# Performance work log

Measured on AMD Instinct MI355X. Metric: run time of the kernel, lower is better.

The kernel has to match this reference:

```python
import jax, jax.numpy as jnp
import numpy as np

B, T, E = 2, 2048, 2048
H, HKV, D = 32, 8, 64
G = H // HKV  # groups = 4
ROPE_BASE = 10000.0


def setup_inputs() -> dict:
    key = jax.random.key(0)
    ks = jax.random.split(key, 5)
    s = 0.02
    return {
        "x": jax.random.normal(ks[0], (B, T, E), dtype=jnp.float32),
        "Wq": jax.random.normal(ks[1], (E, H * D), dtype=jnp.float32) * s,
        "Wk": jax.random.normal(ks[2], (E, HKV * D), dtype=jnp.float32) * s,
        "Wv": jax.random.normal(ks[3], (E, HKV * D), dtype=jnp.float32) * s,
        "Wo": jax.random.normal(ks[4], (E, E), dtype=jnp.float32) * s,
    }


def _rope_tables(t, d, dtype):
    # standard rotate-half RoPE, theta base 10000
    inv_freq = 1.0 / (ROPE_BASE ** (jnp.arange(0, d, 2, dtype=jnp.float32) / d))
    ang = jnp.arange(t, dtype=jnp.float32)[:, None] * inv_freq[None, :]  # [T, D/2]
    return jnp.cos(ang).astype(dtype), jnp.sin(ang).astype(dtype)


def _apply_rope(x, cos, sin):
    # x: [B, h, T, D]; cos/sin: [T, D/2]
    d2 = x.shape[-1] // 2
    x1, x2 = x[..., :d2], x[..., d2:]
    return jnp.concatenate([x1 * cos - x2 * sin, x2 * cos + x1 * sin], axis=-1)


def reference(x, Wq, Wk, Wv, Wo):
    b, t, _ = x.shape
    q = (x @ Wq).reshape(b, t, H, D).transpose(0, 2, 1, 3)      # [B,H,T,D]
    k = (x @ Wk).reshape(b, t, HKV, D).transpose(0, 2, 1, 3)    # [B,HKV,T,D]
    v = (x @ Wv).reshape(b, t, HKV, D).transpose(0, 2, 1, 3)    # [B,HKV,T,D]

    cos, sin = _rope_tables(t, D, x.dtype)
    q = _apply_rope(q, cos, sin)
    k = _apply_rope(k, cos, sin)

    # GQA: keep KV unexpanded, broadcast groups inside the contraction
    qg = q.reshape(b, HKV, G, t, D)
    scale = 1.0 / np.sqrt(D)
    scores = jnp.einsum('bkgtd,bksd->bkgts', qg, k) * scale      # [B,HKV,G,T,T]
    causal = jnp.tril(jnp.ones((t, t), dtype=bool))
    scores = jnp.where(causal, scores, jnp.finfo(scores.dtype).min)
    attn = jax.nn.softmax(scores, axis=-1)
    y = jnp.einsum('bkgts,bksd->bkgtd', attn, v)                 # [B,HKV,G,T,D]
    y = y.reshape(b, H, t, D).transpose(0, 2, 1, 3).reshape(b, t, H * D)
    return y @ Wo
```

## Files before the change

### kernel.cpp

```cpp
#include <hip/hip_runtime.h>
#include <hip/hip_bf16.h>
#include <cstdint>
#include <cstddef>

typedef __bf16 bf16;
typedef __attribute__((ext_vector_type(8))) __bf16 bf16x8;
typedef __attribute__((ext_vector_type(4))) __bf16 bf16x4v;
typedef __attribute__((ext_vector_type(4))) float f32x4;

#define NB 2
#define NT 2048
#define NE 2048
#define NH 32
#define NHKV 8
#define ND 64
#define NBT (NB * NT)
#define NQKV 3072

__device__ __forceinline__ void gload_lds16(const void* g, void* l) {
  __builtin_amdgcn_global_load_lds(
      (const __attribute__((address_space(1))) unsigned int*)g,
      (__attribute__((address_space(3))) unsigned int*)l, 16, 0, 0);
}

__device__ __forceinline__ int swz(int row, int byteoff) {
  return (row * 128 + byteoff) ^ ((row & 7) << 4);
}


__global__ __launch_bounds__(256)
void prep_kernel(const float* __restrict__ x, const float* __restrict__ Wq,
                 const float* __restrict__ Wk, const float* __restrict__ Wv,
                 const float* __restrict__ Wo, bf16* __restrict__ xb,
                 bf16* __restrict__ wqkv_t, bf16* __restrict__ wo_t,
                 float* __restrict__ tab) {
  const int bid = blockIdx.x, tid = threadIdx.x;

  if (bid < 1024) {
    const int n4 = NBT * NE / 4;
    for (int i = bid * 256 + tid; i < n4; i += 1024 * 256) {
      const float4 v = ((const float4*)x)[i];
      bf16x4v o;
      o[0] = (bf16)v.x; o[1] = (bf16)v.y; o[2] = (bf16)v.z; o[3] = (bf16)v.w;
      ((bf16x4v*)xb)[i] = o;
    }
    return;
  }
  if (bid < 1280) {
    const int i = (bid - 1024) * 256 + tid;
    const int t = i >> 5, d = i & 31;
    const float inv = expf(-(float)d * 0.28782313662425574f);
    const float ang = (float)t * inv;
    tab[t * 64 + d] = cosf(ang);
    tab[t * 64 + 32 + d] = sinf(ang);
    return;
  }

  __shared__ float tile[32][33];
  const float* in;
  bf16* outp;
  int ncols, rowoff, gx, sub;
  if (bid < 5376)      { sub = bid - 1280; in = Wq; outp = wqkv_t; ncols = 2048; rowoff = 0;    gx = 64; }
  else if (bid < 6400) { sub = bid - 5376; in = Wk; outp = wqkv_t; ncols = 512;  rowoff = 2048; gx = 16; }
  else if (bid < 7424) { sub = bid - 6400; in = Wv; outp = wqkv_t; ncols = 512;  rowoff = 2560; gx = 16; }
  else                 { sub = bid - 7424; in = Wo; outp = wo_t;   ncols = 2048; rowoff = 0;    gx = 64; }
  const int c0 = (sub % gx) * 32, k0 = (sub / gx) * 32;
  const int tx = tid & 31, ty = tid >> 5;
#pragma unroll
  for (int j = 0; j < 4; ++j)
    tile[ty + j * 8][tx] = in[(size_t)(k0 + ty + j * 8) * ncols + c0 + tx];
  __syncthreads();
#pragma unroll
  for (int j = 0; j < 4; ++j)
    outp[(size_t)(rowoff + c0 + ty + j * 8) * 2048 + k0 + tx] = (bf16)tile[tx][ty + j * 8];
}


template <typename CT, bool ROPE>
__global__ __launch_bounds__(256, 3)
void gemm_r3_kernel(const bf16* __restrict__ A, const bf16* __restrict__ Bt,
                    CT* __restrict__ C, int M, int N, int K,
                    const float* __restrict__ tab, bf16* __restrict__ vt) {
  __shared__ __align__(16) bf16 As[3][128 * 32];
  __shared__ __align__(16) bf16 Bs[3][128 * 32];
  const int tid = threadIdx.x;
  const int lane = tid & 63, wid = tid >> 6;
  const int wr = wid >> 1, wc = wid & 1;
  const int cpx = (int)gridDim.x >> 3;
  const int swzb = ((int)blockIdx.x & 7) * cpx + ((int)blockIdx.x >> 3);
  const int gx = N >> 7;
  const int bx = swzb % gx, by = swzb / gx;
  const int m0 = by * 128, n0 = bx * 128;
  const int srow = tid >> 2;
  const int skoff = 8 * ((tid & 3) ^ ((tid >> 3) & 3));
  const bf16* ga = A + (size_t)(m0 + srow) * K + skoff;
  const bf16* gb = Bt + (size_t)(n0 + srow) * K + skoff;
  const int fr = lane & 15;
  const int fq = lane >> 4;
  const int fks = 8 * (fq ^ ((fr >> 1) & 3));
  const int NTK = K >> 5;
  f32x4 acc[4][4] = {};

#define STAGE_T(b, t)                                                   \
  do {                                                                  \
    const int kk = (t) * 32;                                            \
    gload_lds16(ga + kk, &As[b][tid * 8]);                              \
    gload_lds16(ga + kk + (size_t)64 * K, &As[b][2048 + tid * 8]);      \
    gload_lds16(gb + kk, &Bs[b][tid * 8]);                              \
    gload_lds16(gb + kk + (size_t)64 * K, &Bs[b][2048 + tid * 8]);      \
  } while (0)

  STAGE_T(0, 0);
  STAGE_T(1, 1);

  int bc = 0;
  for (int t = 0; t < NTK; ++t) {
    if (t + 1 < NTK) asm volatile("s_waitcnt vmcnt(4)" ::: "memory");
    else             asm volatile("s_waitcnt vmcnt(0)" ::: "memory");
    __builtin_amdgcn_s_barrier();

    bf16x8 af[4], bfr[4];
#pragma unroll
    for (int m = 0; m < 4; ++m)
      af[m] = *(const bf16x8*)&As[bc][(wr * 64 + m * 16 + fr) * 32 + fks];
#pragma unroll
    for (int n = 0; n < 4; ++n)
      bfr[n] = *(const bf16x8*)&Bs[bc][(wc * 64 + n * 16 + fr) * 32 + fks];

    if (t + 2 < NTK) {
      const int pb = (bc + 2 >= 3) ? bc - 1 : bc + 2;
      STAGE_T(pb, t + 2);
    }

    __builtin_amdgcn_s_setprio(1);
#pragma unroll
    for (int m = 0; m < 4; ++m)
#pragma unroll
      for (int n = 0; n < 4; ++n)
        acc[m][n] = __builtin_amdgcn_mfma_f32_16x16x32_bf16(af[m], bfr[n], acc[m][n], 0, 0, 0);
    __builtin_amdgcn_s_setprio(0);
    bc = (bc + 1 == 3) ? 0 : bc + 1;
  }
#undef STAGE_T

  const int colbase = n0 + wc * 64;

  if (ROPE && colbase >= 2560) {
    const int hk = (colbase - 2560) >> 6;
    const int bb = m0 >> 11;
    const int t0 = (m0 & (NT - 1)) + wr * 64 + fq * 4;
    bf16* vtp = vt + (size_t)(bb * NHKV + hk) * 64 * NT;
#pragma unroll
    for (int m = 0; m < 4; ++m) {
#pragma unroll
      for (int n = 0; n < 4; ++n) {
        const int d = n * 16 + fr;
        bf16x4v w;
        w[0] = (bf16)acc[m][n][0];
        w[1] = (bf16)acc[m][n][1];
        w[2] = (bf16)acc[m][n][2];
        w[3] = (bf16)acc[m][n][3];
        *(bf16x4v*)&vtp[(size_t)d * NT + t0 + m * 16] = w;
      }
    }
    return;
  }

  const bool do_rope = ROPE && colbase < 2560;
  const bool do_scale = ROPE && colbase < 2048;
  const float SCALE = 0.18033688011112042f;
  const int orow0 = m0 + wr * 64 + fq * 4;
  const int ocol0 = colbase + fr;
#pragma unroll
  for (int m = 0; m < 4; ++m) {
#pragma unroll
    for (int j = 0; j < 4; ++j) {
      const int row = orow0 + m * 16 + j;
      float v0 = acc[m][0][j], v1 = acc[m][1][j], v2 = acc[m][2][j], v3 = acc[m][3][j];
      if (do_rope) {
        const int tt = row & (NT - 1);
        const float c0 = tab[tt * 64 + fr],      s0 = tab[tt * 64 + 32 + fr];
        const float c1 = tab[tt * 64 + 16 + fr], s1 = tab[tt * 64 + 48 + fr];
        const float a0 = v0, a2 = v2;
        v0 = a0 * c0 - a2 * s0;
        v2 = a2 * c0 + a0 * s0;
        const float a1 = v1, a3 = v3;
        v1 = a1 * c1 - a3 * s1;
        v3 = a3 * c1 + a1 * s1;
        if (do_scale) { v0 *= SCALE; v1 *= SCALE; v2 *= SCALE; v3 *= SCALE; }
      }
      CT* cp = &C[(size_t)row * N + ocol0];
      cp[0] = (CT)v0; cp[16] = (CT)v1; cp[32] = (CT)v2; cp[48] = (CT)v3;
    }
  }
}


__global__ __launch_bounds__(256, 3)
void attn_kernel(const bf16* __restrict__ qkv, const bf16* __restrict__ vt,
                 bf16* __restrict__ y) {
  const int bid = blockIdx.x;
  const int qtb = 15 - (bid >> 6);
  const int bh = bid & 63;
  const int b = bh >> 5, h = bh & 31, hk = h >> 2;
  const int q0 = qtb * 128;

  __shared__ __align__(16) bf16 Kb[2][4096], Vb[2][4096];

  const int tid = threadIdx.x;
  const int lane = tid & 63, wid = tid >> 6;
  const int ql = lane & 15;
  const int sub = lane >> 4;

  const int st_r = tid >> 3;
  const int kperm = 4 * (st_r >> 4) + 8 * ((st_r >> 2) & 3) + (st_r & 3);
  const int csw = ((tid & 7) ^ (st_r & 7)) * 8;
  const bf16* kgbase = qkv + (size_t)(b * NT + kperm) * NQKV + 2048 + hk * 64 + csw;
  const bf16* vgbase = vt + ((size_t)(b * NHKV + hk) * 64 + st_r) * NT + csw;

  auto STAGE = [&](int buf, int kv0) {
    const bf16* kg = kgbase + (size_t)kv0 * NQKV;
    gload_lds16(kg, Kb[buf] + tid * 8);
    gload_lds16(kg + (size_t)32 * NQKV, Kb[buf] + 2048 + tid * 8);
    const bf16* vg = vgbase + kv0;
    gload_lds16(vg, Vb[buf] + tid * 8);
    gload_lds16(vg + 32 * NT, Vb[buf] + 2048 + tid * 8);
  };

  bf16x8 qf[2][2];
#pragma unroll
  for (int set = 0; set < 2; ++set) {
    const bf16* qp = qkv + (size_t)(b * NT + q0 + wid * 32 + set * 16 + ql) * NQKV + h * 64 + sub * 8;
    qf[set][0] = *(const bf16x8*)qp;
    qf[set][1] = *(const bf16x8*)(qp + 32);
  }

  bf16x8 ones8;
#pragma unroll
  for (int i = 0; i < 8; ++i) ones8[i] = (bf16)1.0f;

  f32x4 o[2][4] = {};
  f32x4 ol[2] = {};
  float m_s[2] = {-1e30f, -1e30f};

  const int ntiles = 2 * qtb + 2;
  STAGE(0, 0);

  for (int it = 0; it < ntiles; ++it) {
    const int kv0 = it * 64;
    const int bc = it & 1;
    asm volatile("s_waitcnt vmcnt(0)" ::: "memory");
    __builtin_amdgcn_s_barrier();
    if (it + 1 < ntiles) STAGE(bc ^ 1, kv0 + 64);

    if (kv0 <= q0 + wid * 32 + 47) {
      bf16x8 kf[4][2];
#pragma unroll
      for (int n = 0; n < 4; ++n)
#pragma unroll
        for (int c = 0; c < 2; ++c)
          kf[n][c] = *(const bf16x8*)((const char*)Kb[bc] + swz(n * 16 + ql, c * 64 + sub * 16));
      bf16x8 vf[2][4];
#pragma unroll
      for (int kc = 0; kc < 2; ++kc)
#pragma unroll
        for (int dt = 0; dt < 4; ++dt)
          vf[kc][dt] = *(const bf16x8*)((const char*)Vb[bc] + swz(dt * 16 + ql, kc * 64 + sub * 16));

#pragma unroll
      for (int set = 0; set < 2; ++set) {
        const int qlo = q0 + wid * 32 + set * 16;
        if (kv0 > qlo + 15) continue;

        f32x4 s[4] = {};
        __builtin_amdgcn_s_setprio(1);
#pragma unroll
        for (int n = 0; n < 4; ++n) {
          s[n] = __builtin_amdgcn_mfma_f32_16x16x32_bf16(kf[n][0], qf[set][0], s[n], 0, 0, 0);
          s[n] = __builtin_amdgcn_mfma_f32_16x16x32_bf16(kf[n][1], qf[set][1], s[n], 0, 0, 0);
        }
        __builtin_amdgcn_s_setprio(0);

        float p[4][4];
        if (kv0 + 63 > qlo) {
          const int qrow = qlo + ql;
#pragma unroll
          for (int n = 0; n < 4; ++n) {
            const int kvb = kv0 + 32 * (n >> 1) + 4 * (n & 1) + 8 * sub;
#pragma unroll
            for (int j = 0; j < 4; ++j)
              p[n][j] = (kvb + j > qrow) ? -1e30f : s[n][j];
          }
        } else {
#pragma unroll
          for (int n = 0; n < 4; ++n)
#pragma unroll
            for (int j = 0; j < 4; ++j)
              p[n][j] = s[n][j];
        }

        float pmax = p[0][0];
#pragma unroll
        for (int n = 0; n < 4; ++n)
#pragma unroll
          for (int j = 0; j < 4; ++j) pmax = fmaxf(pmax, p[n][j]);

        if (!__all(pmax <= m_s[set] + 8.0f)) {
          float rmax = pmax;
          rmax = fmaxf(rmax, __shfl_xor(rmax, 16));
          rmax = fmaxf(rmax, __shfl_xor(rmax, 32));
          const float mnew = fmaxf(m_s[set], rmax);
          const float sc = exp2f(m_s[set] - mnew);
          m_s[set] = mnew;
          ol[set] *= sc;
#pragma unroll
          for (int dt = 0; dt < 4; ++dt) o[set][dt] *= sc;
        }
        const float mcur = m_s[set];

        bf16x8 pb2[2];
#pragma unroll
        for (int n = 0; n < 4; ++n)
#pragma unroll
          for (int j = 0; j < 4; ++j)
            pb2[n >> 1][(n & 1) * 4 + j] = (bf16)exp2f(p[n][j] - mcur);

        __builtin_amdgcn_s_setprio(1);
#pragma unroll
        for (int kc = 0; kc < 2; ++kc) {
          ol[set] = __builtin_amdgcn_mfma_f32_16x16x32_bf16(ones8, pb2[kc], ol[set], 0, 0, 0);
#pragma unroll
          for (int dt = 0; dt < 4; ++dt)
            o[set][dt] = __builtin_amdgcn_mfma_f32_16x16x32_bf16(vf[kc][dt], pb2[kc], o[set][dt], 0, 0, 0);
        }
        __builtin_amdgcn_s_setprio(0);
      }
    }
  }

#pragma unroll
  for (int set = 0; set < 2; ++set) {
    const float inv = 1.0f / ol[set][0];
    bf16* yp = y + (size_t)(b * NT + q0 + wid * 32 + set * 16 + ql) * NE + h * 64 + sub * 4;
#pragma unroll
    for (int dt = 0; dt < 4; ++dt) {
      bf16x4v w;
      w[0] = (bf16)(o[set][dt][0] * inv);
      w[1] = (bf16)(o[set][dt][1] * inv);
      w[2] = (bf16)(o[set][dt][2] * inv);
      w[3] = (bf16)(o[set][dt][3] * inv);
      *(bf16x4v*)(yp + dt * 16) = w;
    }
  }
}


extern "C" void kernel_launch(void* const* d_in, const int* in_sizes, int n_in,
                              void* d_out, int out_size, void* d_ws, size_t ws_size,
                              hipStream_t stream) {
  const float* x = (const float*)d_in[0];
  const float* Wq = (const float*)d_in[1];
  const float* Wk = (const float*)d_in[2];
  const float* Wv = (const float*)d_in[3];
  const float* Wo = (const float*)d_in[4];
  float* out = (float*)d_out;

  char* ws = (char*)d_ws;
  size_t off = 0;
  auto alloc = [&](size_t bytes) -> void* {
    void* p = ws + off;
    off += (bytes + 255) & ~(size_t)255;
    return p;
  };
  bf16* xb = (bf16*)alloc((size_t)NBT * NE * 2);
  bf16* wqkv_t = (bf16*)alloc((size_t)NQKV * NE * 2);
  bf16* wo_t = (bf16*)alloc((size_t)NE * NE * 2);
  bf16* qkv = (bf16*)alloc((size_t)NBT * NQKV * 2);
  bf16* vtb = (bf16*)alloc((size_t)NB * NHKV * ND * NT * 2);
  bf16* yb = (bf16*)alloc((size_t)NBT * NE * 2);
  float* tab = (float*)alloc((size_t)NT * 64 * 4);

  prep_kernel<<<11520, 256, 0, stream>>>(x, Wq, Wk, Wv, Wo, xb, wqkv_t, wo_t, tab);
  gemm_r3_kernel<bf16, true><<<dim3((NQKV / 128) * (NBT / 128)), 256, 0, stream>>>(
      xb, wqkv_t, qkv, NBT, NQKV, NE, tab, vtb);
  attn_kernel<<<dim3(NT / 128 * 64), 256, 0, stream>>>(qkv, vtb, yb);
  gemm_r3_kernel<float, false><<<dim3((NE / 128) * (NBT / 128)), 256, 0, stream>>>(
      yb, wo_t, out, NBT, NE, NE, nullptr, nullptr);
}
```

Baseline: 187.4 us.

## Pair complementary causal query tiles per attention block for balanced work

Each attention block now processes two query tiles, (15-p) and p, in sequence, so every block does the same number of KV tiles. The grid is halved to 512 blocks. The KV staging pipeline runs continuously across the phase boundary, with the accumulators flushed and reset between the two tiles. This removes the causal load imbalance and tail effects, at the cost of fewer resident blocks per CU than the launch bounds allow.

```diff
diff --git a/kernel.cpp b/kernel.cpp
--- a/kernel.cpp
+++ b/kernel.cpp
@@ -200,10 +200,12 @@
 void attn_kernel(const bf16* __restrict__ qkv, const bf16* __restrict__ vt,
                  bf16* __restrict__ y) {
   const int bid = blockIdx.x;
-  const int qtb = 15 - (bid >> 6);
+  const int pidx = bid >> 6;
   const int bh = bid & 63;
   const int b = bh >> 5, h = bh & 31, hk = h >> 2;
-  const int q0 = qtb * 128;
+  const int q0A = (15 - pidx) * 128;
+  const int q0B = pidx * 128;
+  const int ntA = 2 * (15 - pidx) + 2;
 
   __shared__ __align__(16) bf16 Kb[2][4096], Vb[2][4096];
 
@@ -228,12 +230,15 @@
   };
 
   bf16x8 qf[2][2];
-#pragma unroll
-  for (int set = 0; set < 2; ++set) {
-    const bf16* qp = qkv + (size_t)(b * NT + q0 + wid * 32 + set * 16 + ql) * NQKV + h * 64 + sub * 8;
-    qf[set][0] = *(const bf16x8*)qp;
-    qf[set][1] = *(const bf16x8*)(qp + 32);
-  }
+  auto LOADQ = [&](int q0) {
+#pragma unroll
+    for (int set = 0; set < 2; ++set) {
+      const bf16* qp = qkv + (size_t)(b * NT + q0 + wid * 32 + set * 16 + ql) * NQKV + h * 64 + sub * 8;
+      qf[set][0] = *(const bf16x8*)qp;
+      qf[set][1] = *(const bf16x8*)(qp + 32);
+    }
+  };
+  LOADQ(q0A);
 
   bf16x8 ones8;
 #pragma unroll
@@ -243,15 +248,36 @@
   f32x4 ol[2] = {};
   float m_s[2] = {-1e30f, -1e30f};
 
-  const int ntiles = 2 * qtb + 2;
+  auto FLUSH = [&](int q0) {
+#pragma unroll
+    for (int set = 0; set < 2; ++set) {
+      const float inv = 1.0f / ol[set][0];
+      bf16* yp = y + (size_t)(b * NT + q0 + wid * 32 + set * 16 + ql) * NE + h * 64 + sub * 4;
+#pragma unroll
+      for (int dt = 0; dt < 4; ++dt) {
+        bf16x4v w;
+        w[0] = (bf16)(o[set][dt][0] * inv);
+        w[1] = (bf16)(o[set][dt][1] * inv);
+        w[2] = (bf16)(o[set][dt][2] * inv);
+        w[3] = (bf16)(o[set][dt][3] * inv);
+        *(bf16x4v*)(yp + dt * 16) = w;
+      }
+    }
+  };
+
   STAGE(0, 0);
 
-  for (int it = 0; it < ntiles; ++it) {
-    const int kv0 = it * 64;
-    const int bc = it & 1;
+  int q0 = q0A;
+  for (int f = 0; f < 34; ++f) {
+    const bool phB = (f >= ntA);
+    const int kv0 = (phB ? f - ntA : f) * 64;
+    const int bc = f & 1;
     asm volatile("s_waitcnt vmcnt(0)" ::: "memory");
     __builtin_amdgcn_s_barrier();
-    if (it + 1 < ntiles) STAGE(bc ^ 1, kv0 + 64);
+    if (f + 1 < 34) {
+      const int nf = f + 1;
+      STAGE(bc ^ 1, (nf >= ntA ? nf - ntA : nf) * 64);
+    }
 
     if (kv0 <= q0 + wid * 32 + 47) {
       bf16x8 kf[4][2];
@@ -336,22 +362,22 @@
         __builtin_amdgcn_s_setprio(0);
       }
     }
-  }
-
-#pragma unroll
-  for (int set = 0; set < 2; ++set) {
-    const float inv = 1.0f / ol[set][0];
-    bf16* yp = y + (size_t)(b * NT + q0 + wid * 32 + set * 16 + ql) * NE + h * 64 + sub * 4;
-#pragma unroll
-    for (int dt = 0; dt < 4; ++dt) {
-      bf16x4v w;
-      w[0] = (bf16)(o[set][dt][0] * inv);
-      w[1] = (bf16)(o[set][dt][1] * inv);
-      w[2] = (bf16)(o[set][dt][2] * inv);
-      w[3] = (bf16)(o[set][dt][3] * inv);
-      *(bf16x4v*)(yp + dt * 16) = w;
-    }
-  }
+
+    if (f == ntA - 1) {
+      FLUSH(q0A);
+#pragma unroll
+      for (int set = 0; set < 2; ++set) {
+#pragma unroll
+        for (int dt = 0; dt < 4; ++dt) o[set][dt] = f32x4{};
+        ol[set] = f32x4{};
+        m_s[set] = -1e30f;
+      }
+      LOADQ(q0B);
+      q0 = q0B;
+    }
+  }
+
+  FLUSH(q0B);
 }
 
 
@@ -383,7 +409,7 @@
   prep_kernel<<<11520, 256, 0, stream>>>(x, Wq, Wk, Wv, Wo, xb, wqkv_t, wo_t, tab);
   gemm_r3_kernel<bf16, true><<<dim3((NQKV / 128) * (NBT / 128)), 256, 0, stream>>>(
       xb, wqkv_t, qkv, NBT, NQKV, NE, tab, vtb);
-  attn_kernel<<<dim3(NT / 128 * 64), 256, 0, stream>>>(qkv, vtb, yb);
+  attn_kernel<<<dim3(8 * 64), 256, 0, stream>>>(qkv, vtb, yb);
   gemm_r3_kernel<float, false><<<dim3((NE / 128) * (NBT / 128)), 256, 0, stream>>>(
       yb, wo_t, out, NBT, NE, NE, nullptr, nullptr);
 }
```

Measured after the change: 202.7 us. 8.2% more time.
